# Kernel optimization log

Measured on AMD Instinct MI355X. Metric: run time of the kernel, lower is better.

Reference implementation:

```python
import jax, jax.numpy as jnp
import numpy as np

B_, L_, D_, R_, N_ = 8, 1024, 512, 32, 16  # batch, seq(in_channels), dim(=dim_inner), dt_rank, d_state


def setup_inputs() -> dict:
    key = jax.random.key(0)
    ks = jax.random.split(key, 8)
    s = lambda k, shape, scale: jax.random.normal(k, shape, dtype=jnp.float32) * scale
    inv = D_ ** -0.5
    return {
        "x": jax.random.uniform(ks[0], (B_, L_, D_), dtype=jnp.float32),
        "W1": s(ks[1], (D_, D_), inv), "b1": jnp.zeros((D_,), jnp.float32),
        "W2": s(ks[2], (D_, D_), inv), "b2": jnp.zeros((D_,), jnp.float32),
        "Wout": s(ks[3], (D_, D_), inv), "bout": jnp.zeros((D_,), jnp.float32),
        "conv_w": s(ks[4], (L_, L_, 3), (3 * L_) ** -0.5),  # Conv1d(L_, L_, k=3) weight (O,I,W)
        "conv_b": jnp.zeros((L_,), jnp.float32),
        "W_dbc": s(ks[5], (R_ + 2 * N_, D_), inv),          # deltaBC projection (no bias)
        "W_dt": s(ks[6], (D_, R_), R_ ** -0.5),             # dt_proj weight
        "b_dt": jnp.zeros((D_,), jnp.float32),
        "A_log": jnp.log(jnp.tile(jnp.arange(1, N_ + 1, dtype=jnp.float32), (D_, 1))),  # (D, N)
        "Dp": jnp.ones((D_,), jnp.float32),
    }


def _silu(v):
    return v * jax.nn.sigmoid(v)


def _selective_scan(u, delta, A, Bm, Cm, Dp):
    # u, delta: (b, l, d); A: (d, n); Bm, Cm: (b, l, n); Dp: (d,)
    dA = jnp.exp(jnp.einsum('bld,dn->bldn', delta, A))          # (b,l,d,n)
    dBu = jnp.einsum('bld,bln,bld->bldn', delta, Bm, u)          # (b,l,d,n)

    def step(h, inp):
        dA_t, dBu_t, C_t = inp                                   # (b,d,n),(b,d,n),(b,n)
        h = dA_t * h + dBu_t
        return h, jnp.einsum('bdn,bn->bd', h, C_t)

    h0 = jnp.zeros((u.shape[0], u.shape[2], A.shape[1]), u.dtype)
    _, ys = jax.lax.scan(step, h0, (dA.transpose(1, 0, 2, 3), dBu.transpose(1, 0, 2, 3), Cm.transpose(1, 0, 2)))
    return ys.transpose(1, 0, 2) + u * Dp                        # (b,l,d)


def reference(x, W1, b1, W2, b2, Wout, bout, conv_w, conv_b, W_dbc, W_dt, b_dt, A_log, Dp):
    skip = x
    x1 = x @ W1.T + b1                                            # proj_one
    x2 = x @ W2.T + b2                                            # proj_two
    # Conv1d over channel axis = L_ (dim 1), spatial axis = D_ (dim 2)
    x1 = jax.lax.conv_general_dilated(x1, conv_w, window_strides=(1,), padding=((1, 1),),
                                      dimension_numbers=('NCW', 'OIW', 'NCW')) + conv_b[None, :, None]
    x1 = _silu(x1)
    # SSM (zeta-style): deltaBC -> split -> dt_proj -> softplus -> selective scan
    dbc = x1 @ W_dbc.T                                            # (b,l,R+2N)
    delta = jax.nn.softplus(dbc[..., :R_] @ W_dt.T + b_dt)        # (b,l,d)
    Bm, Cm = dbc[..., R_:R_ + N_], dbc[..., R_ + N_:]
    A = -jnp.exp(A_log)
    y = _selective_scan(x1, delta, A, Bm, Cm, Dp)
    out = y * _silu(x2) + skip
    return out @ Wout.T + bout
```

## Files before the change

### kernel.cpp

```cpp
#include <hip/hip_runtime.h>
#include <hip/hip_bf16.h>

typedef __hip_bfloat16 bf16;
typedef __bf16 bf16x8 __attribute__((ext_vector_type(8)));
typedef float f32x4 __attribute__((ext_vector_type(4)));

static_assert(sizeof(bf16) == 2, "bf16 must be 2 bytes");

#define NC 32
#define CH 32
#define X1TP_BSTRIDE (514L * 1024)

__device__ __forceinline__ float silu_f(float v) { return v / (1.0f + __expf(-v)); }

__device__ __forceinline__ void gload16(const bf16* g, bf16* l) {
  __builtin_amdgcn_global_load_lds((const __attribute__((address_space(1))) void*)g,
                                   (__attribute__((address_space(3))) void*)l,
                                   16, 0, 0);
}

__global__ __launch_bounds__(256) void f2b_kernel(const float* __restrict__ in,
                                                  bf16* __restrict__ out, int n) {
  int i = (blockIdx.x * 256 + threadIdx.x) * 4;
  if (i + 3 < n) {
    float4 v = *reinterpret_cast<const float4*>(in + i);
    ushort4 s;
    s.x = __builtin_bit_cast(unsigned short, __float2bfloat16(v.x));
    s.y = __builtin_bit_cast(unsigned short, __float2bfloat16(v.y));
    s.z = __builtin_bit_cast(unsigned short, __float2bfloat16(v.z));
    s.w = __builtin_bit_cast(unsigned short, __float2bfloat16(v.w));
    *reinterpret_cast<ushort4*>(out + i) = s;
  }
}

__global__ __launch_bounds__(256) void csplit_kernel(const float* __restrict__ cw,
                                                     bf16* __restrict__ cws) {
  long idx = (long)blockIdx.x * 256 + threadIdx.x;
  int o = (int)(idx >> 10), i = (int)(idx & 1023);
  float a = cw[idx * 3], b = cw[idx * 3 + 1], c = cw[idx * 3 + 2];
  cws[(long)o * 3072 + i]        = __float2bfloat16(a);
  cws[(long)o * 3072 + 1024 + i] = __float2bfloat16(b);
  cws[(long)o * 3072 + 2048 + i] = __float2bfloat16(c);
}

__global__ __launch_bounds__(256) void zpad_kernel(bf16* __restrict__ x1tp) {
  int e = blockIdx.x * 256 + threadIdx.x;
  int b = e >> 11, rem = e & 2047;
  int r = rem >> 10, i = rem & 1023;
  x1tp[(long)b * X1TP_BSTRIDE + (long)r * (513 * 1024) + i] = __float2bfloat16(0.f);
}

template <int EPI, int BM, int BN, int CONVB>
__global__ __launch_bounds__(256) void gemm_nt(const bf16* __restrict__ A,
                                               const bf16* __restrict__ Bw,
                                               const float* __restrict__ bias,
                                               float* __restrict__ outf,
                                               bf16* __restrict__ outb,
                                               int M, int N, int K,
                                               long sAz, long sBz, long sOz) {
  constexpr int BK = 64;
  constexpr int MI = BM / 32;
  constexpr int WNF = BN / 32;
  constexpr int APW = BM / 32;
  constexpr int BPW = BN / 32;
  __shared__ __align__(16) bf16 As[2][BM * BK];
  __shared__ __align__(16) bf16 Bs[2][BN * BK];

  const int tid = threadIdx.x;
  const int w = tid >> 6, l = tid & 63;
  const int wm = w >> 1, wn = w & 1;
  const int m0 = blockIdx.x * BM, n0 = blockIdx.y * BN;
  const int z = blockIdx.z;
  const bf16* Ab = A + (long)z * sAz + (long)m0 * K;
  const bf16* Bb = Bw + (long)z * sBz;

  const int lrow = l >> 3;
  const int lcol = (((l & 7) ^ (l >> 3)) << 3);

  auto stage = [&](int buf, int k0) {
#pragma unroll
    for (int j = 0; j < APW; ++j) {
      int iss = w * APW + j;
      int row = iss * 8 + lrow;
      gload16(Ab + (long)row * K + k0 + lcol, &As[buf][iss * 512]);
    }
#pragma unroll
    for (int j = 0; j < BPW; ++j) {
      int iss = w * BPW + j;
      int row = iss * 8 + lrow;
      const bf16* src;
      if (CONVB) src = Bb + (long)(n0 + row + (k0 >> 10)) * 1024 + (k0 & 1023) + lcol;
      else       src = Bb + (long)(n0 + row) * K + k0 + lcol;
      gload16(src, &Bs[buf][iss * 512]);
    }
  };

  f32x4 acc[MI][WNF] = {};
  const int nt = K / BK;
  const int lr = l & 15;
  const int lko = (l >> 4) * 8;
  const int xorm = (lr & 7) << 3;

  stage(0, 0);
  for (int t = 0; t < nt; ++t) {
    const int cur = t & 1;
    asm volatile("s_waitcnt vmcnt(0)" ::: "memory");
    __syncthreads();
    if (t + 1 < nt) stage(cur ^ 1, (t + 1) * BK);
#pragma unroll
    for (int kk = 0; kk < 2; ++kk) {
      const int col = (lko + kk * 32) ^ xorm;
      bf16x8 af[MI], bfg[WNF];
#pragma unroll
      for (int mi = 0; mi < MI; ++mi)
        af[mi] = *reinterpret_cast<const bf16x8*>(&As[cur][(wm * (BM / 2) + mi * 16 + lr) * 64 + col]);
#pragma unroll
      for (int ni = 0; ni < WNF; ++ni)
        bfg[ni] = *reinterpret_cast<const bf16x8*>(&Bs[cur][(wn * (BN / 2) + ni * 16 + lr) * 64 + col]);
#pragma unroll
      for (int mi = 0; mi < MI; ++mi)
#pragma unroll
        for (int ni = 0; ni < WNF; ++ni)
          acc[mi][ni] = __builtin_amdgcn_mfma_f32_16x16x32_bf16(af[mi], bfg[ni], acc[mi][ni], 0, 0, 0);
    }
  }

  const int lq = l >> 4;
#pragma unroll
  for (int mi = 0; mi < MI; ++mi) {
#pragma unroll
    for (int ni = 0; ni < WNF; ++ni) {
#pragma unroll
      for (int j = 0; j < 4; ++j) {
        int m = m0 + wm * (BM / 2) + mi * 16 + lq * 4 + j;
        int n = n0 + wn * (BN / 2) + ni * 16 + lr;
        float v = acc[mi][ni][j];
        if (EPI == 2) {
          v += bias[m];
          (outb + (long)z * sOz)[(long)m * N + n] = __float2bfloat16(silu_f(v));
        } else if (EPI == 3) {
          outf[(long)m * N + n] = v;
        } else if (EPI == 4) {
          v += bias[n];
          outf[(long)m * N + n] = v;
        } else {
          v += bias[m];
          int b = n >> 10, li = n & 1023;
          outb[(long)b * X1TP_BSTRIDE + (long)(m + 1) * 1024 + li] = __float2bfloat16(v);
        }
      }
    }
  }
}

__global__ __launch_bounds__(256) void scan_p1(const bf16* __restrict__ u_bf,
                                               const float* __restrict__ dbc,
                                               const float* __restrict__ W_dt,
                                               const float* __restrict__ b_dt,
                                               const float* __restrict__ A_log,
                                               float* __restrict__ P,
                                               float* __restrict__ Q) {
  const int tid = threadIdx.x;
  const int d = blockIdx.x * 256 + tid;
  const int c = blockIdx.y, b = blockIdx.z;
  __shared__ float sD[CH][64];
  for (int i = tid; i < CH * 64; i += 256) {
    int tt = i >> 6, j = i & 63;
    sD[tt][j] = dbc[((long)b * 1024 + c * CH + tt) * 64 + j];
  }
  __syncthreads();
  float wdt[32];
#pragma unroll
  for (int r = 0; r < 32; r += 4) {
    float4 v = *reinterpret_cast<const float4*>(&W_dt[(long)d * 32 + r]);
    wdt[r] = v.x; wdt[r + 1] = v.y; wdt[r + 2] = v.z; wdt[r + 3] = v.w;
  }
  const float bd = b_dt[d];
  float Adn[16];
#pragma unroll
  for (int n = 0; n < 16; ++n) Adn[n] = -__expf(A_log[d * 16 + n]);
  float p[16], q[16];
#pragma unroll
  for (int n = 0; n < 16; ++n) { p[n] = 1.f; q[n] = 0.f; }
  const long rowb = (long)b * 1024 + c * CH;
  for (int tt = 0; tt < CH; ++tt) {
    float a = bd;
#pragma unroll
    for (int r = 0; r < 32; ++r) a = fmaf(sD[tt][r], wdt[r], a);
    float dv = fmaxf(a, 0.f) + log1pf(__expf(-fabsf(a)));
    float uv = __bfloat162float(u_bf[(rowb + tt) * 512 + d]);
    float s = dv * uv;
#pragma unroll
    for (int n = 0; n < 16; ++n) {
      float dA = __expf(dv * Adn[n]);
      p[n] *= dA;
      q[n] = fmaf(dA, q[n], s * sD[tt][32 + n]);
    }
  }
  float* Pp = P + ((long)b * NC + c) * 8192 + (long)d * 16;
  float* Qp = Q + ((long)b * NC + c) * 8192 + (long)d * 16;
#pragma unroll
  for (int n4 = 0; n4 < 4; ++n4) {
    *reinterpret_cast<float4*>(Pp + n4 * 4) = make_float4(p[n4*4], p[n4*4+1], p[n4*4+2], p[n4*4+3]);
    *reinterpret_cast<float4*>(Qp + n4 * 4) = make_float4(q[n4*4], q[n4*4+1], q[n4*4+2], q[n4*4+3]);
  }
}

__global__ __launch_bounds__(256) void scan_p2(const float* __restrict__ P,
                                               const float* __restrict__ Q,
                                               float* __restrict__ Hin) {
  const int dn = blockIdx.x * 256 + threadIdx.x;
  const int b = blockIdx.y;
  float h = 0.f;
#pragma unroll 4
  for (int c = 0; c < NC; ++c) {
    long idx = ((long)b * NC + c) * 8192 + dn;
    Hin[idx] = h;
    h = fmaf(P[idx], h, Q[idx]);
  }
}

__global__ __launch_bounds__(256) void scan_p3(const bf16* __restrict__ u_bf,
                                               const float* __restrict__ dbc,
                                               const float* __restrict__ W_dt,
                                               const float* __restrict__ b_dt,
                                               const float* __restrict__ A_log,
                                               const float* __restrict__ Dp,
                                               const float* __restrict__ x2s,
                                               const float* __restrict__ x,
                                               const float* __restrict__ Hin,
                                               bf16* __restrict__ zb) {
  const int tid = threadIdx.x;
  const int d = blockIdx.x * 256 + tid;
  const int c = blockIdx.y, b = blockIdx.z;
  __shared__ float sD[CH][64];
  for (int i = tid; i < CH * 64; i += 256) {
    int tt = i >> 6, j = i & 63;
    sD[tt][j] = dbc[((long)b * 1024 + c * CH + tt) * 64 + j];
  }
  __syncthreads();
  float wdt[32];
#pragma unroll
  for (int r = 0; r < 32; r += 4) {
    float4 v = *reinterpret_cast<const float4*>(&W_dt[(long)d * 32 + r]);
    wdt[r] = v.x; wdt[r + 1] = v.y; wdt[r + 2] = v.z; wdt[r + 3] = v.w;
  }
  const float bd = b_dt[d];
  float Adn[16];
#pragma unroll
  for (int n = 0; n < 16; ++n) Adn[n] = -__expf(A_log[d * 16 + n]);
  float h[16];
  const float* Hp = Hin + ((long)b * NC + c) * 8192 + (long)d * 16;
#pragma unroll
  for (int n4 = 0; n4 < 4; ++n4) {
    float4 v = *reinterpret_cast<const float4*>(Hp + n4 * 4);
    h[n4*4] = v.x; h[n4*4+1] = v.y; h[n4*4+2] = v.z; h[n4*4+3] = v.w;
  }
  const float Dpv = Dp[d];
  const long rowb = (long)b * 1024 + c * CH;
  for (int tt = 0; tt < CH; ++tt) {
    long off = (rowb + tt) * 512 + d;
    float a = bd;
#pragma unroll
    for (int r = 0; r < 32; ++r) a = fmaf(sD[tt][r], wdt[r], a);
    float dv = fmaxf(a, 0.f) + log1pf(__expf(-fabsf(a)));
    float uv = __bfloat162float(u_bf[off]);
    float s = dv * uv;
    float y = uv * Dpv;
#pragma unroll
    for (int n = 0; n < 16; ++n) {
      float dA = __expf(dv * Adn[n]);
      h[n] = fmaf(dA, h[n], s * sD[tt][32 + n]);
      y = fmaf(h[n], sD[tt][48 + n], y);
    }
    float zv = fmaf(y, silu_f(x2s[off]), x[off]);
    zb[off] = __float2bfloat16(zv);
  }
}

extern "C" void kernel_launch(void* const* d_in, const int* in_sizes, int n_in,
                              void* d_out, int out_size, void* d_ws, size_t ws_size,
                              hipStream_t stream) {
  (void)in_sizes; (void)n_in; (void)out_size; (void)ws_size;
  const float* x    = (const float*)d_in[0];
  const float* W1   = (const float*)d_in[1];
  const float* b1   = (const float*)d_in[2];
  const float* W2   = (const float*)d_in[3];
  const float* b2   = (const float*)d_in[4];
  const float* Wout = (const float*)d_in[5];
  const float* bout = (const float*)d_in[6];
  const float* convw = (const float*)d_in[7];
  const float* convb = (const float*)d_in[8];
  const float* Wdbc = (const float*)d_in[9];
  const float* Wdt  = (const float*)d_in[10];
  const float* bdt  = (const float*)d_in[11];
  const float* Alog = (const float*)d_in[12];
  const float* Dp   = (const float*)d_in[13];
  float* out = (float*)d_out;

  char* ws = (char*)d_ws;
  size_t off = 0;
  auto alloc = [&](size_t bytes) { void* p = ws + off; off += (bytes + 255) & ~(size_t)255; return p; };
  bf16* xb     = (bf16*)alloc(8192L * 512 * 2);
  bf16* w1b    = (bf16*)alloc(512L * 512 * 2);
  bf16* w2b    = (bf16*)alloc(512L * 512 * 2);
  bf16* woutb  = (bf16*)alloc(512L * 512 * 2);
  bf16* wdbcb  = (bf16*)alloc(64L * 512 * 2);
  bf16* cws    = (bf16*)alloc(1024L * 3072 * 2);
  bf16* x1tp   = (bf16*)alloc(8L * X1TP_BSTRIDE * 2);
  float* x2s   = (float*)alloc(8192L * 512 * 4);
  bf16* x1s    = (bf16*)alloc(8192L * 512 * 2);
  float* dbc   = (float*)alloc(8192L * 64 * 4);
  float* P     = (float*)alloc(8L * NC * 8192 * 4);
  float* Q     = (float*)alloc(8L * NC * 8192 * 4);
  float* Hin   = (float*)alloc(8L * NC * 8192 * 4);
  bf16* zb = xb;

  f2b_kernel<<<8192 * 512 / 1024, 256, 0, stream>>>(x, xb, 8192 * 512);
  f2b_kernel<<<512 * 512 / 1024, 256, 0, stream>>>(W1, w1b, 512 * 512);
  f2b_kernel<<<512 * 512 / 1024, 256, 0, stream>>>(W2, w2b, 512 * 512);
  f2b_kernel<<<512 * 512 / 1024, 256, 0, stream>>>(Wout, woutb, 512 * 512);
  f2b_kernel<<<64 * 512 / 1024, 256, 0, stream>>>(Wdbc, wdbcb, 64 * 512);
  csplit_kernel<<<1024 * 1024 / 256, 256, 0, stream>>>(convw, cws);
  zpad_kernel<<<64, 256, 0, stream>>>(x1tp);

  gemm_nt<5, 64, 128, 0><<<dim3(8, 64, 1), 256, 0, stream>>>(
      w1b, xb, b1, nullptr, x1tp, 512, 8192, 512, 0, 0, 0);
  gemm_nt<4, 64, 128, 0><<<dim3(128, 4, 1), 256, 0, stream>>>(
      xb, w2b, b2, x2s, nullptr, 8192, 512, 512, 0, 0, 0);
  gemm_nt<2, 64, 128, 1><<<dim3(16, 4, 8), 256, 0, stream>>>(
      cws, x1tp, convb, nullptr, x1s, 1024, 512, 3072, 0, X1TP_BSTRIDE, 1024L * 512);
  gemm_nt<3, 64, 64, 0><<<dim3(128, 1, 1), 256, 0, stream>>>(
      x1s, wdbcb, nullptr, dbc, nullptr, 8192, 64, 512, 0, 0, 0);
  scan_p1<<<dim3(2, NC, 8), 256, 0, stream>>>(x1s, dbc, Wdt, bdt, Alog, P, Q);
  scan_p2<<<dim3(32, 8, 1), 256, 0, stream>>>(P, Q, Hin);
  scan_p3<<<dim3(2, NC, 8), 256, 0, stream>>>(x1s, dbc, Wdt, bdt, Alog, Dp, x2s, x, Hin, zb);
  gemm_nt<4, 64, 128, 0><<<dim3(128, 4, 1), 256, 0, stream>>>(
      zb, woutb, bout, out, nullptr, 8192, 512, 512, 0, 0, 0);
}
```

Before: 186.7 us.

## Triple-buffer GEMM pipeline, remap blocks across XCDs, fuse prep kernels, bf16 gate

The GEMM moves from double to triple-buffered LDS staging with partial vmcnt waits, so loads for tile t+2 stay in flight during compute. Blocks are remapped through a 1D grid that interleaves across the eight XCDs. The weight conversions and zero-padding are fused into one prep kernel. The x2 projection now applies SiLU in its epilogue and stores bf16, and the scan reads the residual from the bf16 copy of x, cutting memory traffic. In exchange, the gate and residual lose precision to bf16, and xb aliased as zb is read and written in the same scan kernel.

```diff
diff --git a/kernel.cpp b/kernel.cpp
--- a/kernel.cpp
+++ b/kernel.cpp
@@ -17,6 +17,13 @@
   __builtin_amdgcn_global_load_lds((const __attribute__((address_space(1))) void*)g,
                                    (__attribute__((address_space(3))) void*)l,
                                    16, 0, 0);
+}
+
+template <int N> __device__ __forceinline__ void wait_vm() {
+  if constexpr (N == 0)      asm volatile("s_waitcnt vmcnt(0)" ::: "memory");
+  else if constexpr (N == 4) asm volatile("s_waitcnt vmcnt(4)" ::: "memory");
+  else if constexpr (N == 6) asm volatile("s_waitcnt vmcnt(6)" ::: "memory");
+  else static_assert(N == 0 || N == 4 || N == 6, "add case");
 }
 
 __global__ __launch_bounds__(256) void f2b_kernel(const float* __restrict__ in,
@@ -33,6 +40,35 @@
   }
 }
 
+__global__ __launch_bounds__(256) void prep_kernel(const float* __restrict__ W1,
+                                                   const float* __restrict__ W2,
+                                                   const float* __restrict__ Wout,
+                                                   const float* __restrict__ Wdbc,
+                                                   bf16* __restrict__ w1b, bf16* __restrict__ w2b,
+                                                   bf16* __restrict__ woutb, bf16* __restrict__ wdbcb,
+                                                   bf16* __restrict__ x1tp) {
+  int gid = blockIdx.x * 256 + threadIdx.x;
+  int i = gid * 4;
+  auto cvt4 = [&](const float* src, bf16* dst) {
+    float4 v = *reinterpret_cast<const float4*>(src + i);
+    ushort4 s;
+    s.x = __builtin_bit_cast(unsigned short, __float2bfloat16(v.x));
+    s.y = __builtin_bit_cast(unsigned short, __float2bfloat16(v.y));
+    s.z = __builtin_bit_cast(unsigned short, __float2bfloat16(v.z));
+    s.w = __builtin_bit_cast(unsigned short, __float2bfloat16(v.w));
+    *reinterpret_cast<ushort4*>(dst + i) = s;
+  };
+  cvt4(W1, w1b);
+  cvt4(W2, w2b);
+  cvt4(Wout, woutb);
+  if (i < 64 * 512) cvt4(Wdbc, wdbcb);
+  if (gid < 16384) {
+    int b = gid >> 11, rem = gid & 2047;
+    int r = rem >> 10, ii = rem & 1023;
+    x1tp[(long)b * X1TP_BSTRIDE + (long)r * (513 * 1024) + ii] = __float2bfloat16(0.f);
+  }
+}
+
 __global__ __launch_bounds__(256) void csplit_kernel(const float* __restrict__ cw,
                                                      bf16* __restrict__ cws) {
   long idx = (long)blockIdx.x * 256 + threadIdx.x;
@@ -43,14 +79,7 @@
   cws[(long)o * 3072 + 2048 + i] = __float2bfloat16(c);
 }
 
-__global__ __launch_bounds__(256) void zpad_kernel(bf16* __restrict__ x1tp) {
-  int e = blockIdx.x * 256 + threadIdx.x;
-  int b = e >> 11, rem = e & 2047;
-  int r = rem >> 10, i = rem & 1023;
-  x1tp[(long)b * X1TP_BSTRIDE + (long)r * (513 * 1024) + i] = __float2bfloat16(0.f);
-}
-
-template <int EPI, int BM, int BN, int CONVB>
+template <int EPI, int BM, int BN, int CONVB, int GX, int GY>
 __global__ __launch_bounds__(256) void gemm_nt(const bf16* __restrict__ A,
                                                const bf16* __restrict__ Bw,
                                                const float* __restrict__ bias,
@@ -59,18 +88,21 @@
                                                int M, int N, int K,
                                                long sAz, long sBz, long sOz) {
   constexpr int BK = 64;
-  constexpr int MI = BM / 32;
-  constexpr int WNF = BN / 32;
-  constexpr int APW = BM / 32;
-  constexpr int BPW = BN / 32;
-  __shared__ __align__(16) bf16 As[2][BM * BK];
-  __shared__ __align__(16) bf16 Bs[2][BN * BK];
+  constexpr int MI = BM / 32, WNF = BN / 32;
+  constexpr int APW = BM / 32, BPW = BN / 32;
+  constexpr int IPW = APW + BPW;
+  __shared__ __align__(16) bf16 As[3][BM * BK];
+  __shared__ __align__(16) bf16 Bs[3][BN * BK];
+
+  const int bid = (blockIdx.x & 7) * ((int)gridDim.x >> 3) + (blockIdx.x >> 3);
+  const int bx = bid & (GX - 1);
+  const int by = (bid / GX) & (GY - 1);
+  const int z  = bid / (GX * GY);
 
   const int tid = threadIdx.x;
   const int w = tid >> 6, l = tid & 63;
   const int wm = w >> 1, wn = w & 1;
-  const int m0 = blockIdx.x * BM, n0 = blockIdx.y * BN;
-  const int z = blockIdx.z;
+  const int m0 = bx * BM, n0 = by * BN;
   const bf16* Ab = A + (long)z * sAz + (long)m0 * K;
   const bf16* Bb = Bw + (long)z * sBz;
 
@@ -102,11 +134,13 @@
   const int xorm = (lr & 7) << 3;
 
   stage(0, 0);
+  stage(1, BK);
   for (int t = 0; t < nt; ++t) {
-    const int cur = t & 1;
-    asm volatile("s_waitcnt vmcnt(0)" ::: "memory");
-    __syncthreads();
-    if (t + 1 < nt) stage(cur ^ 1, (t + 1) * BK);
+    const int cur = t % 3;
+    if (t + 1 < nt) wait_vm<IPW>();
+    else            wait_vm<0>();
+    __builtin_amdgcn_s_barrier();
+    __builtin_amdgcn_sched_barrier(0);
 #pragma unroll
     for (int kk = 0; kk < 2; ++kk) {
       const int col = (lko + kk * 32) ^ xorm;
@@ -123,6 +157,9 @@
         for (int ni = 0; ni < WNF; ++ni)
           acc[mi][ni] = __builtin_amdgcn_mfma_f32_16x16x32_bf16(af[mi], bfg[ni], acc[mi][ni], 0, 0, 0);
     }
+    __builtin_amdgcn_sched_barrier(0);
+    __builtin_amdgcn_s_barrier();
+    if (t + 2 < nt) stage((t + 2) % 3, (t + 2) * BK);
   }
 
   const int lq = l >> 4;
@@ -143,10 +180,13 @@
         } else if (EPI == 4) {
           v += bias[n];
           outf[(long)m * N + n] = v;
-        } else {
+        } else if (EPI == 5) {
           v += bias[m];
           int b = n >> 10, li = n & 1023;
           outb[(long)b * X1TP_BSTRIDE + (long)(m + 1) * 1024 + li] = __float2bfloat16(v);
+        } else {
+          v += bias[n];
+          outb[(long)m * N + n] = __float2bfloat16(silu_f(v));
         }
       }
     }
@@ -226,8 +266,8 @@
                                                const float* __restrict__ b_dt,
                                                const float* __restrict__ A_log,
                                                const float* __restrict__ Dp,
-                                               const float* __restrict__ x2s,
-                                               const float* __restrict__ x,
+                                               const bf16* __restrict__ x2g,
+                                               const bf16* __restrict__ xres,
                                                const float* __restrict__ Hin,
                                                bf16* __restrict__ zb) {
   const int tid = threadIdx.x;
@@ -273,8 +313,9 @@
       h[n] = fmaf(dA, h[n], s * sD[tt][32 + n]);
       y = fmaf(h[n], sD[tt][48 + n], y);
     }
-    float zv = fmaf(y, silu_f(x2s[off]), x[off]);
-    zb[off] = __float2bfloat16(zv);
+    float gate = __bfloat162float(x2g[off]);
+    float xv = __bfloat162float(xres[off]);
+    zb[off] = __float2bfloat16(fmaf(y, gate, xv));
   }
 }
 
@@ -308,7 +349,7 @@
   bf16* wdbcb  = (bf16*)alloc(64L * 512 * 2);
   bf16* cws    = (bf16*)alloc(1024L * 3072 * 2);
   bf16* x1tp   = (bf16*)alloc(8L * X1TP_BSTRIDE * 2);
-  float* x2s   = (float*)alloc(8192L * 512 * 4);
+  bf16* x2g    = (bf16*)alloc(8192L * 512 * 2);
   bf16* x1s    = (bf16*)alloc(8192L * 512 * 2);
   float* dbc   = (float*)alloc(8192L * 64 * 4);
   float* P     = (float*)alloc(8L * NC * 8192 * 4);
@@ -317,24 +358,20 @@
   bf16* zb = xb;
 
   f2b_kernel<<<8192 * 512 / 1024, 256, 0, stream>>>(x, xb, 8192 * 512);
-  f2b_kernel<<<512 * 512 / 1024, 256, 0, stream>>>(W1, w1b, 512 * 512);
-  f2b_kernel<<<512 * 512 / 1024, 256, 0, stream>>>(W2, w2b, 512 * 512);
-  f2b_kernel<<<512 * 512 / 1024, 256, 0, stream>>>(Wout, woutb, 512 * 512);
-  f2b_kernel<<<64 * 512 / 1024, 256, 0, stream>>>(Wdbc, wdbcb, 64 * 512);
+  prep_kernel<<<256, 256, 0, stream>>>(W1, W2, Wout, Wdbc, w1b, w2b, woutb, wdbcb, x1tp);
   csplit_kernel<<<1024 * 1024 / 256, 256, 0, stream>>>(convw, cws);
-  zpad_kernel<<<64, 256, 0, stream>>>(x1tp);
-
-  gemm_nt<5, 64, 128, 0><<<dim3(8, 64, 1), 256, 0, stream>>>(
+
+  gemm_nt<5, 64, 128, 0, 8, 64><<<512, 256, 0, stream>>>(
       w1b, xb, b1, nullptr, x1tp, 512, 8192, 512, 0, 0, 0);
-  gemm_nt<4, 64, 128, 0><<<dim3(128, 4, 1), 256, 0, stream>>>(
-      xb, w2b, b2, x2s, nullptr, 8192, 512, 512, 0, 0, 0);
-  gemm_nt<2, 64, 128, 1><<<dim3(16, 4, 8), 256, 0, stream>>>(
+  gemm_nt<6, 64, 128, 0, 128, 4><<<512, 256, 0, stream>>>(
+      xb, w2b, b2, nullptr, x2g, 8192, 512, 512, 0, 0, 0);
+  gemm_nt<2, 64, 128, 1, 16, 4><<<512, 256, 0, stream>>>(
       cws, x1tp, convb, nullptr, x1s, 1024, 512, 3072, 0, X1TP_BSTRIDE, 1024L * 512);
-  gemm_nt<3, 64, 64, 0><<<dim3(128, 1, 1), 256, 0, stream>>>(
+  gemm_nt<3, 64, 64, 0, 128, 1><<<128, 256, 0, stream>>>(
       x1s, wdbcb, nullptr, dbc, nullptr, 8192, 64, 512, 0, 0, 0);
   scan_p1<<<dim3(2, NC, 8), 256, 0, stream>>>(x1s, dbc, Wdt, bdt, Alog, P, Q);
   scan_p2<<<dim3(32, 8, 1), 256, 0, stream>>>(P, Q, Hin);
-  scan_p3<<<dim3(2, NC, 8), 256, 0, stream>>>(x1s, dbc, Wdt, bdt, Alog, Dp, x2s, x, Hin, zb);
-  gemm_nt<4, 64, 128, 0><<<dim3(128, 4, 1), 256, 0, stream>>>(
+  scan_p3<<<dim3(2, NC, 8), 256, 0, stream>>>(x1s, dbc, Wdt, bdt, Alog, Dp, x2g, xb, Hin, zb);
+  gemm_nt<4, 64, 128, 0, 128, 4><<<512, 256, 0, stream>>>(
       zb, woutb, bout, out, nullptr, 8192, 512, 512, 0, 0, 0);
 }
```

Measured after the change: 177.7 us. 1.05x faster.
